# Kernel tuning notes

Measured on AMD Instinct MI355X. Metric: run time of the kernel, lower is better.

The kernel has to match this reference:

```python
import jax, jax.numpy as jnp
import numpy as np

B, L, D = 64, 128, 768          # batch, padded seq len, bert dim
H, HA = 1024, 256               # d_label_hidden, d_label_hidden_arc
POS, V = 18, 40                 # pos vocab, arc (deprel) vocab


def setup_inputs() -> dict:
    key = jax.random.key(0)
    ks = jax.random.split(key, 24)
    n = lambda i, shape, s=0.02: jax.random.normal(ks[i], shape, jnp.float32) * s
    # realistic padding: random sentence lengths in [L//2, L]
    lengths = jax.random.randint(ks[1], (B,), L // 2, L + 1)
    pad_mask = (jnp.arange(L)[None, :] < lengths[:, None]).astype(jnp.float32)
    heads = jax.random.randint(ks[2], (B, L), 0, L)
    # mark padded positions as -1 (zero head vector), as in the original loop
    heads = jnp.where(pad_mask > 0, heads, -1)
    return {
        "ann": jax.random.normal(ks[0], (B, L, D), jnp.float32),
        "pad_mask": pad_mask,
        "correct_heads": heads,
        # label-biaffine branch (hidden H)
        "W_head_mlp": n(3, (D, H)), "b_head_mlp": n(4, (H,)),
        "W_dep_mlp": n(5, (D, H)), "b_dep_mlp": n(6, (H,)),
        "W_lin": n(7, (H, H)), "b_lin": n(8, (H,)),
        "head_vec": n(9, (H,), 1.0), "dep_vec": n(10, (H,), 1.0),
        "bias": n(11, (1, 1, 1), 1.0),
        # arc-label biaffine branch (hidden HA, per-label bilinear)
        "W_head_arc_mlp": n(12, (D, HA)), "b_head_arc_mlp": n(13, (HA,)),
        "W_dep_arc_mlp": n(14, (D, HA)), "b_dep_arc_mlp": n(15, (HA,)),
        "W_arc": n(16, (V, HA, HA), 1.0),
        "head_vec_arc": n(17, (HA, V), 1.0), "dep_vec_arc": n(18, (HA, V), 1.0),
        "bias_arc": n(19, (1, 1, V), 1.0),
        # POS tip
        "W_pos": n(20, (D, POS)), "b_pos": n(21, (POS,)),
    }


def reference(ann, pad_mask, correct_heads,
              W_head_mlp, b_head_mlp, W_dep_mlp, b_dep_mlp,
              W_lin, b_lin, head_vec, dep_vec, bias,
              W_head_arc_mlp, b_head_arc_mlp, W_dep_arc_mlp, b_dep_arc_mlp,
              W_arc, head_vec_arc, dep_vec_arc, bias_arc,
              W_pos, b_pos):
    # POS prediction
    pos_pred = ann @ W_pos + b_pos                                  # [B,L,POS]

    # ---- dependency (unlabeled arc) biaffine ----
    ann_head = jax.nn.relu(ann @ W_head_mlp + b_head_mlp)           # [B,L,H]
    ann_dep = jax.nn.relu(ann @ W_dep_mlp + b_dep_mlp)              # [B,L,H]
    head_bias = ann_head @ head_vec                                 # [B,L]
    dep_bias = ann_dep @ dep_vec                                    # [B,L]
    Wh = ann_head @ W_lin + b_lin                                   # [B,L,H]
    # scores[b,i,j] = dep[b,i] . Wh[b,j]
    dep_W_headT = jnp.einsum('bih,bjh->bij', ann_dep, Wh)
    dep_W_headT = dep_W_headT + head_bias[:, None, :] + dep_bias[:, :, None] + bias
    valid_head = pad_mask[:, None, :] > 0                           # [B,1,L]
    dep_W_headT = jnp.where(valid_head, dep_W_headT, -jnp.inf)

    # ---- labeled arc biaffine (gather gold head per dependent) ----
    ann_head_arc = jax.nn.relu(ann @ W_head_arc_mlp + b_head_arc_mlp)  # [B,L,HA]
    ann_dep_arc = jax.nn.relu(ann @ W_dep_arc_mlp + b_dep_arc_mlp)     # [B,L,HA]
    idx = jnp.clip(correct_heads, 0, L - 1)
    gathered = jnp.take_along_axis(ann_head_arc, idx[:, :, None], axis=1)
    gathered = jnp.where((correct_heads == -1)[:, :, None], 0.0, gathered)  # [B,L,HA]

    head_arc_bias = gathered @ head_vec_arc                         # [B,L,V]
    dep_arc_bias = ann_dep_arc @ dep_vec_arc                        # [B,L,V]
    # per-label bilinear: s[b,l,v] = gathered[b,l] . W_arc[v] . dep[b,l]
    dep_W_headT_arc = jnp.einsum('bld,vde,ble->blv', gathered, W_arc, ann_dep_arc)
    dep_W_headT_arc = dep_W_headT_arc + head_arc_bias + dep_arc_bias + bias_arc

    return pos_pred, dep_W_headT, dep_W_headT_arc
```

## Files before the change

kernel.cpp:

```cpp
#include <hip/hip_runtime.h>
#include <hip/hip_bf16.h>

#define B_ 64
#define L_ 128
#define D_ 768
#define H_ 1024
#define HA_ 256
#define POS_ 18
#define V_ 40
#define BL_ (B_ * L_)

#define NEG_BIG (-1.0e30f)

typedef __attribute__((ext_vector_type(8))) short short8v;
typedef __attribute__((ext_vector_type(4))) short short4v;
typedef __attribute__((ext_vector_type(4))) float f32x4;

__device__ inline void split_bf16(float x, short& hi, short& lo) {
  __hip_bfloat16 h = __float2bfloat16(x);
  hi = *reinterpret_cast<short*>(&h);
  const float r = x - __bfloat162float(h);
  __hip_bfloat16 l = __float2bfloat16(r);
  lo = *reinterpret_cast<short*>(&l);
}

__device__ __forceinline__ short f2b(float x) {
  __hip_bfloat16 h = __float2bfloat16(x);
  return *reinterpret_cast<short*>(&h);
}
__device__ __forceinline__ float b2f(short s) {
  __hip_bfloat16 h = *reinterpret_cast<__hip_bfloat16*>(&s);
  return __bfloat162float(h);
}

__device__ __forceinline__ int swz8(int row, int s) { return ((s + (row >> 1)) & 3) * 8; }
__device__ __forceinline__ int colswz(int row, int n) {
  return (n & ~31) + swz8(row, (n >> 3) & 3) + (n & 7);
}

__device__ __forceinline__ void ld_lds16(const void* g, void* l) {
  __builtin_amdgcn_global_load_lds(
      (const __attribute__((address_space(1))) unsigned int*)g,
      (__attribute__((address_space(3))) unsigned int*)l, 16, 0, 0);
}

template<bool RELU, bool HASBIAS>
__global__ __launch_bounds__(256)
void gemm_bias(const float* __restrict__ A, const float* __restrict__ Bm,
               const float* __restrict__ bias, float* __restrict__ C,
               int M, int N, int K) {
  __shared__ __align__(16) float As[16][68];
  __shared__ __align__(16) float Bs[16][68];
  const int t = threadIdx.x;
  const int tx = t & 15, ty = t >> 4;
  const int m0 = blockIdx.y * 64, n0 = blockIdx.x * 64;
  const int arow = t >> 2, aks = (t & 3) * 4;
  const int bkr = t >> 4, bns = (t & 15) * 4;
  float acc[4][4] = {};
  for (int k0 = 0; k0 < K; k0 += 16) {
    const float4 av = *reinterpret_cast<const float4*>(&A[(size_t)(m0 + arow) * K + k0 + aks]);
    float4 bv;
    const int nb = n0 + bns;
    if (nb + 3 < N) {
      bv = *reinterpret_cast<const float4*>(&Bm[(size_t)(k0 + bkr) * N + nb]);
    } else {
      bv.x = (nb + 0 < N) ? Bm[(size_t)(k0 + bkr) * N + nb + 0] : 0.f;
      bv.y = (nb + 1 < N) ? Bm[(size_t)(k0 + bkr) * N + nb + 1] : 0.f;
      bv.z = (nb + 2 < N) ? Bm[(size_t)(k0 + bkr) * N + nb + 2] : 0.f;
      bv.w = 0.f;
    }
    __syncthreads();
    As[aks + 0][arow] = av.x;
    As[aks + 1][arow] = av.y;
    As[aks + 2][arow] = av.z;
    As[aks + 3][arow] = av.w;
    *reinterpret_cast<float4*>(&Bs[bkr][bns]) = bv;
    __syncthreads();
#pragma unroll
    for (int kk = 0; kk < 16; ++kk) {
      const float4 a4 = *reinterpret_cast<const float4*>(&As[kk][ty * 4]);
      const float4 b4 = *reinterpret_cast<const float4*>(&Bs[kk][tx * 4]);
      const float aa[4] = {a4.x, a4.y, a4.z, a4.w};
      const float bb[4] = {b4.x, b4.y, b4.z, b4.w};
#pragma unroll
      for (int i = 0; i < 4; ++i)
#pragma unroll
        for (int j = 0; j < 4; ++j)
          acc[i][j] = fmaf(aa[i], bb[j], acc[i][j]);
    }
  }
#pragma unroll
  for (int j = 0; j < 4; ++j) {
    const int n = n0 + tx * 4 + j;
    if (n >= N) continue;
    float bj = 0.f;
    if constexpr (HASBIAS) bj = bias[n];
#pragma unroll
    for (int i = 0; i < 4; ++i) {
      const int m = m0 + ty * 4 + i;
      float v = acc[i][j] + bj;
      if (RELU) v = fmaxf(v, 0.f);
      C[(size_t)m * N + n] = v;
    }
  }
}

__global__ __launch_bounds__(256)
void split_pre(const float* __restrict__ src, short* __restrict__ hi,
               short* __restrict__ lo, int K) {
  const int t = threadIdx.x;
  const int r = blockIdx.x * 4 + (t >> 6);
  const int lane = t & 63;
  for (int c = lane * 4; c < K; c += 256) {
    const float4 v = *reinterpret_cast<const float4*>(&src[(size_t)r * K + c]);
    const float vv[4] = {v.x, v.y, v.z, v.w};
    short4v h4, l4;
#pragma unroll
    for (int j = 0; j < 4; ++j) {
      short h, l;
      split_bf16(vv[j], h, l);
      h4[j] = h; l4[j] = l;
    }
    const int cs = colswz(r, c);
    *reinterpret_cast<short4v*>(&hi[(size_t)r * K + cs]) = h4;
    *reinterpret_cast<short4v*>(&lo[(size_t)r * K + cs]) = l4;
  }
}

__global__ __launch_bounds__(256)
void transpose_h(const float* __restrict__ W, short* __restrict__ Thi,
                 int K, int N) {
  __shared__ float tile[32][33];
  const int k0 = blockIdx.y * 32, n0 = blockIdx.x * 32;
  const int t = threadIdx.x;
  const int r = t >> 3, c = (t & 7) * 4;
  const float4 w4 = *reinterpret_cast<const float4*>(&W[(size_t)(k0 + r) * N + n0 + c]);
  tile[r][c + 0] = w4.x;
  tile[r][c + 1] = w4.y;
  tile[r][c + 2] = w4.z;
  tile[r][c + 3] = w4.w;
  __syncthreads();
  short4v hi4;
#pragma unroll
  for (int j = 0; j < 4; ++j) hi4[j] = f2b(tile[c + j][r]);
  const int row = n0 + r;
  const int cs = swz8(row, (c >> 3) & 3) + (c & 7);
  *reinterpret_cast<short4v*>(&Thi[(size_t)row * K + k0 + cs]) = hi4;
}

__global__ __launch_bounds__(256)
void transpose_pos(const float* __restrict__ W, short* __restrict__ Th,
                   short* __restrict__ Tl) {
  const int t = threadIdx.x;
  const int k0 = blockIdx.x * 32;
  const int n = t & 31;
  const int ks = (t >> 5) * 4;
#pragma unroll
  for (int j = 0; j < 4; ++j) {
    const int k = k0 + ks + j;
    const float v = (n < POS_) ? W[(size_t)k * POS_ + n] : 0.f;
    short h, l;
    split_bf16(v, h, l);
    Th[(size_t)n * D_ + colswz(n, k)] = h;
    Tl[(size_t)n * D_ + colswz(n, k)] = l;
  }
}

__global__ __launch_bounds__(256)
void transpose_dv(const float* __restrict__ dv, float* __restrict__ dvT) {
  const int v = blockIdx.x;
  const int e = threadIdx.x;
  dvT[(size_t)v * HA_ + e] = dv[(size_t)e * V_ + v];
}

template<bool STOREBF>
__global__ __launch_bounds__(256)
void gemm_h2(const short* __restrict__ Ath,
             const short* __restrict__ B1t, const short* __restrict__ B2t,
             const float* __restrict__ bias1v, const float* __restrict__ bias2v,
             void* __restrict__ O1, void* __restrict__ O2,
             int M, int N, int K) {
  __shared__ __align__(16) short AhP[2][4096];
  __shared__ __align__(16) short B1P[2][4096];
  __shared__ __align__(16) short B2P[2][4096];
  const int t = threadIdx.x;
  const int lane = t & 63, w = t >> 6;
  const int wm = w >> 1, wn = w & 1;
  const int m0 = blockIdx.y * 128, n0 = blockIdx.x * 128;
  const int fr = lane & 15, kgi = lane >> 4;
  const int drow = lane >> 2, dslot = lane & 3;
  f32x4 acc1[4][4] = {};
  f32x4 acc2[4][4] = {};
  const int nt = K >> 5;

  auto stage = [&](int tt, int pb) {
    const int k0 = tt << 5;
#pragma unroll
    for (int cc = 0; cc < 2; ++cc) {
      const int c = w * 2 + cc;
      const size_t ga = (size_t)(m0 + c * 16 + drow) * K + k0 + dslot * 8;
      ld_lds16(&Ath[ga], &AhP[pb][c * 512]);
      const size_t gb = (size_t)(n0 + c * 16 + drow) * K + k0 + dslot * 8;
      ld_lds16(&B1t[gb], &B1P[pb][c * 512]);
      ld_lds16(&B2t[gb], &B2P[pb][c * 512]);
    }
  };
  auto compute = [&](int pb) {
    short8v ah[4];
#pragma unroll
    for (int mi = 0; mi < 4; ++mi) {
      const int r = wm * 64 + mi * 16 + fr;
      ah[mi] = *reinterpret_cast<const short8v*>(&AhP[pb][r * 32 + swz8(r, kgi)]);
    }
    __builtin_amdgcn_s_setprio(1);
#pragma unroll
    for (int nj = 0; nj < 4; ++nj) {
      const int rn = wn * 64 + nj * 16 + fr;
      const int sw = swz8(rn, kgi);
      const short8v b1 = *reinterpret_cast<const short8v*>(&B1P[pb][rn * 32 + sw]);
      const short8v b2 = *reinterpret_cast<const short8v*>(&B2P[pb][rn * 32 + sw]);
#pragma unroll
      for (int mi = 0; mi < 4; ++mi) {
        acc1[mi][nj] = __builtin_amdgcn_mfma_f32_16x16x32_bf16(ah[mi], b1, acc1[mi][nj], 0, 0, 0);
        acc2[mi][nj] = __builtin_amdgcn_mfma_f32_16x16x32_bf16(ah[mi], b2, acc2[mi][nj], 0, 0, 0);
      }
    }
    __builtin_amdgcn_s_setprio(0);
  };

  stage(0, 0);
  int cur = 0;
  for (int tt = 0; tt < nt; ++tt) {
    if (tt + 1 < nt) {
      stage(tt + 1, cur ^ 1);
      asm volatile("s_waitcnt vmcnt(6)" ::: "memory");
    } else {
      asm volatile("s_waitcnt vmcnt(0)" ::: "memory");
    }
    __builtin_amdgcn_s_barrier();
    compute(cur);
    __builtin_amdgcn_s_barrier();
    cur ^= 1;
  }

  const int rg = lane >> 4;
#pragma unroll
  for (int nj = 0; nj < 4; ++nj) {
    const int n = n0 + wn * 64 + nj * 16 + fr;
    const float b1 = bias1v[n];
    const float b2 = bias2v[n];
#pragma unroll
    for (int mi = 0; mi < 4; ++mi) {
#pragma unroll
      for (int q = 0; q < 4; ++q) {
        const int m = m0 + wm * 64 + mi * 16 + rg * 4 + q;
        float v1 = fmaxf(acc1[mi][nj][q] + b1, 0.f);
        float v2 = fmaxf(acc2[mi][nj][q] + b2, 0.f);
        if constexpr (STOREBF) {
          const size_t o = (size_t)m * N + colswz(m, n);
          ((short*)O1)[o] = f2b(v1);
          ((short*)O2)[o] = f2b(v2);
        } else {
          ((float*)O1)[(size_t)m * N + n] = v1;
          ((float*)O2)[(size_t)m * N + n] = v2;
        }
      }
    }
  }
}

template<bool RELU>
__global__ __launch_bounds__(256)
void gemm_hs(const short* __restrict__ Ath, const short* __restrict__ Bth,
             const float* __restrict__ bias, short* __restrict__ Oh,
             int M, int N, int K) {
  __shared__ __align__(16) short AhP[2][4096];
  __shared__ __align__(16) short BhP[2][4096];
  const int t = threadIdx.x;
  const int lane = t & 63, w = t >> 6;
  const int wm = w >> 1, wn = w & 1;
  const int m0 = blockIdx.y * 128, n0 = blockIdx.x * 128;
  const int fr = lane & 15, kgi = lane >> 4;
  const int drow = lane >> 2, dslot = lane & 3;
  f32x4 acc[4][4] = {};
  const int nt = K >> 5;

  auto stage = [&](int tt, int pb) {
    const int k0 = tt << 5;
#pragma unroll
    for (int cc = 0; cc < 2; ++cc) {
      const int c = w * 2 + cc;
      const size_t ga = (size_t)(m0 + c * 16 + drow) * K + k0 + dslot * 8;
      ld_lds16(&Ath[ga], &AhP[pb][c * 512]);
      const size_t gb = (size_t)(n0 + c * 16 + drow) * K + k0 + dslot * 8;
      ld_lds16(&Bth[gb], &BhP[pb][c * 512]);
    }
  };
  auto compute = [&](int pb) {
    short8v ah[4];
#pragma unroll
    for (int mi = 0; mi < 4; ++mi) {
      const int r = wm * 64 + mi * 16 + fr;
      ah[mi] = *reinterpret_cast<const short8v*>(&AhP[pb][r * 32 + swz8(r, kgi)]);
    }
    __builtin_amdgcn_s_setprio(1);
#pragma unroll
    for (int nj = 0; nj < 4; ++nj) {
      const int rn = wn * 64 + nj * 16 + fr;
      const short8v bh = *reinterpret_cast<const short8v*>(&BhP[pb][rn * 32 + swz8(rn, kgi)]);
#pragma unroll
      for (int mi = 0; mi < 4; ++mi)
        acc[mi][nj] = __builtin_amdgcn_mfma_f32_16x16x32_bf16(ah[mi], bh, acc[mi][nj], 0, 0, 0);
    }
    __builtin_amdgcn_s_setprio(0);
  };

  stage(0, 0);
  int cur = 0;
  for (int tt = 0; tt < nt; ++tt) {
    if (tt + 1 < nt) {
      stage(tt + 1, cur ^ 1);
      asm volatile("s_waitcnt vmcnt(4)" ::: "memory");
    } else {
      asm volatile("s_waitcnt vmcnt(0)" ::: "memory");
    }
    __builtin_amdgcn_s_barrier();
    compute(cur);
    __builtin_amdgcn_s_barrier();
    cur ^= 1;
  }

  const int rg = lane >> 4;
#pragma unroll
  for (int nj = 0; nj < 4; ++nj) {
    const int n = n0 + wn * 64 + nj * 16 + fr;
    const float bj = bias[n];
#pragma unroll
    for (int mi = 0; mi < 4; ++mi) {
#pragma unroll
      for (int q = 0; q < 4; ++q) {
        const int m = m0 + wm * 64 + mi * 16 + rg * 4 + q;
        float v2 = acc[mi][nj][q] + bj;
        if (RELU) v2 = fmaxf(v2, 0.f);
        Oh[(size_t)m * N + colswz(m, n)] = f2b(v2);
      }
    }
  }
}

__global__ __launch_bounds__(256)
void pos_mfma(const short* __restrict__ Ath, const short* __restrict__ Atl,
              const short* __restrict__ Pth, const short* __restrict__ Ptl,
              const float* __restrict__ bias, float* __restrict__ out) {
  extern __shared__ short sm[];
  short* AhP = sm;
  short* AlP = sm + 16384;
  short* BhP = sm + 32768;
  short* BlP = sm + 34816;
  const int t = threadIdx.x;
  const int m0 = blockIdx.x * 256;
  const int lane = t & 63, w = t >> 6;
  const int fr = lane & 15, kgi = lane >> 4;
  const int drow = lane >> 2, dslot = lane & 3;
  f32x4 acc[4][2] = {};

  auto stage = [&](int tt, int pb) {
    const int k0 = tt << 5;
#pragma unroll
    for (int cc = 0; cc < 4; ++cc) {
      const int c = w * 4 + cc;
      const size_t ga = (size_t)(m0 + c * 16 + drow) * D_ + k0 + dslot * 8;
      ld_lds16(&Ath[ga], &AhP[pb * 8192 + c * 512]);
      ld_lds16(&Atl[ga], &AlP[pb * 8192 + c * 512]);
    }
    {
      const short* bsrc = (w & 2) ? Ptl : Pth;
      short* bdst = (w & 2) ? BlP : BhP;
      const int c = w & 1;
      const size_t gb = (size_t)(c * 16 + drow) * D_ + k0 + dslot * 8;
      ld_lds16(&bsrc[gb], &bdst[pb * 1024 + c * 512]);
    }
  };
  auto compute = [&](int pb) {
    short8v ah[4], al[4];
#pragma unroll
    for (int mi = 0; mi < 4; ++mi) {
      const int r = w * 64 + mi * 16 + fr;
      const int sw = swz8(r, kgi);
      ah[mi] = *reinterpret_cast<const short8v*>(&AhP[pb * 8192 + r * 32 + sw]);
      al[mi] = *reinterpret_cast<const short8v*>(&AlP[pb * 8192 + r * 32 + sw]);
    }
#pragma unroll
    for (int nj = 0; nj < 2; ++nj) {
      const int rn = nj * 16 + fr;
      const int sw = swz8(rn, kgi);
      const short8v bh = *reinterpret_cast<const short8v*>(&BhP[pb * 1024 + rn * 32 + sw]);
      const short8v bl = *reinterpret_cast<const short8v*>(&BlP[pb * 1024 + rn * 32 + sw]);
#pragma unroll
      for (int mi = 0; mi < 4; ++mi) {
        acc[mi][nj] = __builtin_amdgcn_mfma_f32_16x16x32_bf16(ah[mi], bh, acc[mi][nj], 0, 0, 0);
        acc[mi][nj] = __builtin_amdgcn_mfma_f32_16x16x32_bf16(al[mi], bh, acc[mi][nj], 0, 0, 0);
        acc[mi][nj] = __builtin_amdgcn_mfma_f32_16x16x32_bf16(ah[mi], bl, acc[mi][nj], 0, 0, 0);
      }
    }
  };

  stage(0, 0);
  int cur = 0;
  for (int tt = 0; tt < 24; ++tt) {
    if (tt + 1 < 24) {
      stage(tt + 1, cur ^ 1);
      asm volatile("s_waitcnt vmcnt(9)" ::: "memory");
    } else {
      asm volatile("s_waitcnt vmcnt(0)" ::: "memory");
    }
    __builtin_amdgcn_s_barrier();
    compute(cur);
    __builtin_amdgcn_s_barrier();
    cur ^= 1;
  }

  const int rg = lane >> 4;
#pragma unroll
  for (int nj = 0; nj < 2; ++nj) {
    const int n = nj * 16 + fr;
    if (n >= POS_) continue;
    const float bj = bias[n];
#pragma unroll
    for (int mi = 0; mi < 4; ++mi) {
#pragma unroll
      for (int q = 0; q < 4; ++q) {
        const int m = m0 + w * 64 + mi * 16 + rg * 4 + q;
        out[(size_t)m * POS_ + n] = acc[mi][nj][q] + bj;
      }
    }
  }
}

__global__ __launch_bounds__(256)
void bias_dots_h(const short* __restrict__ Ahh, const short* __restrict__ Adh,
                 const float* __restrict__ head_vec, const float* __restrict__ dep_vec,
                 float* __restrict__ hb, float* __restrict__ db) {
  const int t = threadIdx.x;
  const int m = blockIdx.x * 4 + (t >> 6);
  const int lane = t & 63;
  float sh = 0.f, sd = 0.f;
#pragma unroll
  for (int jj = 0; jj < 4; ++jj) {
    const int c = lane * 16 + jj * 4;
    const size_t o = (size_t)m * H_ + colswz(m, c);
    const short4v h4 = *reinterpret_cast<const short4v*>(&Ahh[o]);
    const short4v d4 = *reinterpret_cast<const short4v*>(&Adh[o]);
    const float4 hv = *reinterpret_cast<const float4*>(&head_vec[c]);
    const float4 dv = *reinterpret_cast<const float4*>(&dep_vec[c]);
    const float hvv[4] = {hv.x, hv.y, hv.z, hv.w};
    const float dvv[4] = {dv.x, dv.y, dv.z, dv.w};
#pragma unroll
    for (int j = 0; j < 4; ++j) {
      sh = fmaf(b2f(h4[j]), hvv[j], sh);
      sd = fmaf(b2f(d4[j]), dvv[j], sd);
    }
  }
#pragma unroll
  for (int off = 32; off; off >>= 1) {
    sh += __shfl_xor(sh, off);
    sd += __shfl_xor(sd, off);
  }
  if (lane == 0) {
    hb[m] = sh;
    db[m] = sd;
  }
}

__global__ __launch_bounds__(256)
void scores_h(const short* __restrict__ Adh, const short* __restrict__ Whh,
              const float* __restrict__ hb, const float* __restrict__ db,
              const float* __restrict__ pad_mask, const float* __restrict__ bias1,
              float* __restrict__ out2) {
  __shared__ __align__(16) short AhP[2][2048];
  __shared__ __align__(16) short BhP[2][2048];
  const int t = threadIdx.x;
  const int b = blockIdx.z;
  const int i0 = blockIdx.y * 64, j0 = blockIdx.x * 64;
  const int lane = t & 63, w = t >> 6;
  const int wm = w >> 1, wn = w & 1;
  const int fr = lane & 15, kgi = lane >> 4;
  const int drow = lane >> 2, dslot = lane & 3;
  const size_t abase = ((size_t)b * L_ + i0) * H_;
  const size_t bbase = ((size_t)b * L_ + j0) * H_;
  f32x4 acc[2][2] = {};

  auto stage = [&](int tt, int pb) {
    const int k0 = tt << 5;
    const size_t ga = abase + (size_t)(w * 16 + drow) * H_ + k0 + dslot * 8;
    ld_lds16(&Adh[ga], &AhP[pb][w * 512]);
    const size_t gb = bbase + (size_t)(w * 16 + drow) * H_ + k0 + dslot * 8;
    ld_lds16(&Whh[gb], &BhP[pb][w * 512]);
  };
  auto compute = [&](int pb) {
    short8v ah[2];
#pragma unroll
    for (int mi = 0; mi < 2; ++mi) {
      const int r = wm * 32 + mi * 16 + fr;
      ah[mi] = *reinterpret_cast<const short8v*>(&AhP[pb][r * 32 + swz8(r, kgi)]);
    }
    __builtin_amdgcn_s_setprio(1);
#pragma unroll
    for (int nj = 0; nj < 2; ++nj) {
      const int rn = wn * 32 + nj * 16 + fr;
      const short8v bh = *reinterpret_cast<const short8v*>(&BhP[pb][rn * 32 + swz8(rn, kgi)]);
#pragma unroll
      for (int mi = 0; mi < 2; ++mi)
        acc[mi][nj] = __builtin_amdgcn_mfma_f32_16x16x32_bf16(ah[mi], bh, acc[mi][nj], 0, 0, 0);
    }
    __builtin_amdgcn_s_setprio(0);
  };

  stage(0, 0);
  int cur = 0;
  for (int tt = 0; tt < 32; ++tt) {
    if (tt + 1 < 32) {
      stage(tt + 1, cur ^ 1);
      asm volatile("s_waitcnt vmcnt(2)" ::: "memory");
    } else {
      asm volatile("s_waitcnt vmcnt(0)" ::: "memory");
    }
    __builtin_amdgcn_s_barrier();
    compute(cur);
    __builtin_amdgcn_s_barrier();
    cur ^= 1;
  }

  const int rg = lane >> 4;
  const float bias0 = bias1[0];
#pragma unroll
  for (int nj = 0; nj < 2; ++nj) {
    const int jcol = j0 + wn * 32 + nj * 16 + fr;
    const float mj = pad_mask[b * L_ + jcol];
    const float hbj = hb[b * L_ + jcol];
#pragma unroll
    for (int mi = 0; mi < 2; ++mi) {
#pragma unroll
      for (int q = 0; q < 4; ++q) {
        const int irow = i0 + wm * 32 + mi * 16 + rg * 4 + q;
        float v = acc[mi][nj][q] + hbj + db[b * L_ + irow] + bias0;
        if (!(mj > 0.f)) v = NEG_BIG;
        out2[((size_t)b * L_ + irow) * L_ + jcol] = v;
      }
    }
  }
}

__global__ __launch_bounds__(256)
void transposeW_h(const float* __restrict__ W, short* __restrict__ Whi) {
  __shared__ float tile[32][33];
  const int v = blockIdx.z, d0 = blockIdx.y * 32, e0 = blockIdx.x * 32;
  const int t = threadIdx.x;
  const int r = t >> 3, c = (t & 7) * 4;
  const float4 w4 = *reinterpret_cast<const float4*>(
      &W[((size_t)v * HA_ + d0 + r) * HA_ + e0 + c]);
  tile[r][c + 0] = w4.x;
  tile[r][c + 1] = w4.y;
  tile[r][c + 2] = w4.z;
  tile[r][c + 3] = w4.w;
  __syncthreads();
  short4v hi4;
#pragma unroll
  for (int j = 0; j < 4; ++j) hi4[j] = f2b(tile[c + j][r]);
  const int row = e0 + r;
  const int cs = swz8(row, (c >> 3) & 3) + (c & 7);
  *reinterpret_cast<short4v*>(&Whi[((size_t)v * HA_ + row) * HA_ + d0 + cs]) = hi4;
}

__global__ __launch_bounds__(256)
void gather_h(const float* __restrict__ head_arcb, const int* __restrict__ heads,
              float* __restrict__ g32, short* __restrict__ g_hi) {
  const int t = threadIdx.x;
  const int m = blockIdx.x * 4 + (t >> 6);
  const int lane = t & 63;
  const int h = heads[m];
  float4 g4 = make_float4(0.f, 0.f, 0.f, 0.f);
  if (h >= 0)
    g4 = *reinterpret_cast<const float4*>(
        &head_arcb[((size_t)((m >> 7) * L_ + h)) * HA_ + lane * 4]);
  *reinterpret_cast<float4*>(&g32[(size_t)m * HA_ + lane * 4]) = g4;
  short4v hi4;
  const float gv[4] = {g4.x, g4.y, g4.z, g4.w};
#pragma unroll
  for (int j = 0; j < 4; ++j) hi4[j] = f2b(gv[j]);
  *reinterpret_cast<short4v*>(&g_hi[(size_t)m * HA_ + colswz(m, lane * 4)]) = hi4;
}

__global__ __launch_bounds__(512)
void arc_h(const short* __restrict__ g_hi, const short* __restrict__ Wt_hi,
           const float* __restrict__ dep32, const float* __restrict__ hb_arc,
           const float* __restrict__ dvT, float* __restrict__ out3) {
  __shared__ __align__(16) short AhP[2][8192];
  __shared__ __align__(16) short BhP[2][8192];
  __shared__ float parts[256][2];
  const int t = threadIdx.x;
  const int bid = blockIdx.x;
  const int xcd = bid & 7;
  const int j = bid >> 3;
  const int m0 = (j / 5) * 256;
  const int v = xcd * 5 + (j % 5);
  const int lane = t & 63, w = t >> 6;
  const int wm = w >> 1, we = w & 1;
  const int fr = lane & 15, kgi = lane >> 4;
  const int drow = lane >> 2, dslot = lane & 3;
  const size_t wbase = (size_t)v * HA_ * HA_;

  f32x4 acc[4][8] = {};

  auto stage = [&](int tt, int pb) {
    const int k0 = tt << 5;
#pragma unroll
    for (int cc = 0; cc < 2; ++cc) {
      const int c = w * 2 + cc;
      const size_t ga = (size_t)(m0 + c * 16 + drow) * HA_ + k0 + dslot * 8;
      ld_lds16(&g_hi[ga], &AhP[pb][c * 512]);
      const size_t gb = wbase + (size_t)(c * 16 + drow) * HA_ + k0 + dslot * 8;
      ld_lds16(&Wt_hi[gb], &BhP[pb][c * 512]);
    }
  };
  auto compute = [&](int pb) {
    short8v ah[4];
#pragma unroll
    for (int mi = 0; mi < 4; ++mi) {
      const int r = wm * 64 + mi * 16 + fr;
      ah[mi] = *reinterpret_cast<const short8v*>(&AhP[pb][r * 32 + swz8(r, kgi)]);
    }
    __builtin_amdgcn_s_setprio(1);
#pragma unroll
    for (int ej = 0; ej < 8; ++ej) {
      const int rb = we * 128 + ej * 16 + fr;
      const short8v bh = *reinterpret_cast<const short8v*>(&BhP[pb][rb * 32 + swz8(rb, kgi)]);
#pragma unroll
      for (int mi = 0; mi < 4; ++mi)
        acc[mi][ej] = __builtin_amdgcn_mfma_f32_16x16x32_bf16(ah[mi], bh, acc[mi][ej], 0, 0, 0);
    }
    __builtin_amdgcn_s_setprio(0);
  };

  stage(0, 0);
  int cur = 0;
#pragma unroll
  for (int tt = 0; tt < 8; ++tt) {
    if (tt < 7) {
      stage(tt + 1, cur ^ 1);
      asm volatile("s_waitcnt vmcnt(4)" ::: "memory");
    } else {
      asm volatile("s_waitcnt vmcnt(0)" ::: "memory");
    }
    __builtin_amdgcn_s_barrier();
    compute(cur);
    __builtin_amdgcn_s_barrier();
    cur ^= 1;
  }

  const int rg = lane >> 4;
  float dvr[8];
#pragma unroll
  for (int ej = 0; ej < 8; ++ej)
    dvr[ej] = dvT[(size_t)v * HA_ + we * 128 + ej * 16 + fr];
#pragma unroll
  for (int mi = 0; mi < 4; ++mi) {
#pragma unroll
    for (int q = 0; q < 4; ++q) {
      const int mrow = wm * 64 + mi * 16 + rg * 4 + q;
      const int m = m0 + mrow;
      float s = 0.f;
#pragma unroll
      for (int ej = 0; ej < 8; ++ej)
        s = fmaf(acc[mi][ej][q] + dvr[ej],
                 dep32[(size_t)m * HA_ + we * 128 + ej * 16 + fr], s);
      s += __shfl_xor(s, 1, 16);
      s += __shfl_xor(s, 2, 16);
      s += __shfl_xor(s, 4, 16);
      s += __shfl_xor(s, 8, 16);
      if (fr == 0) parts[mrow][we] = s;
    }
  }
  __syncthreads();
  if (t < 256) {
    const int m = m0 + t;
    out3[(size_t)m * V_ + v] = parts[t][0] + parts[t][1] + hb_arc[(size_t)m * V_ + v];
  }
}

extern "C" void kernel_launch(void* const* d_in, const int* in_sizes, int n_in,
                              void* d_out, int out_size, void* d_ws, size_t ws_size,
                              hipStream_t stream) {
  const float* ann        = (const float*)d_in[0];
  const float* pad_mask   = (const float*)d_in[1];
  const int*   heads      = (const int*)d_in[2];
  const float* W_head_mlp = (const float*)d_in[3];
  const float* b_head_mlp = (const float*)d_in[4];
  const float* W_dep_mlp  = (const float*)d_in[5];
  const float* b_dep_mlp  = (const float*)d_in[6];
  const float* W_lin      = (const float*)d_in[7];
  const float* b_lin      = (const float*)d_in[8];
  const float* head_vec   = (const float*)d_in[9];
  const float* dep_vec    = (const float*)d_in[10];
  const float* bias1      = (const float*)d_in[11];
  const float* W_head_arc = (const float*)d_in[12];
  const float* b_head_arc = (const float*)d_in[13];
  const float* W_dep_arc  = (const float*)d_in[14];
  const float* b_dep_arc  = (const float*)d_in[15];
  const float* W_arc      = (const float*)d_in[16];
  const float* hv_arc     = (const float*)d_in[17];
  const float* dv_arc     = (const float*)d_in[18];
  const float* bias_arc   = (const float*)d_in[19];
  const float* W_pos      = (const float*)d_in[20];
  const float* b_pos      = (const float*)d_in[21];

  float* out_pos    = (float*)d_out;
  float* out_scores = out_pos + (size_t)BL_ * POS_;
  float* out_arc    = out_scores + (size_t)B_ * L_ * L_;

  float* ws  = (float*)d_ws;
  float* R1  = ws;
  float* R2  = R1 + (size_t)BL_ * H_;
  float* R3  = R2 + (size_t)BL_ * H_;
  float* head_arcb = R3 + (size_t)BL_ * H_;
  float* dep_arcb  = head_arcb + (size_t)BL_ * HA_;
  float* hb        = dep_arcb + (size_t)BL_ * HA_;
  float* db        = hb + BL_;
  short* wt0     = (short*)(db + BL_);
  short* Wth_hm  = wt0;
  short* Wth_dm  = Wth_hm + (size_t)H_ * D_;
  short* Wth_lin = Wth_dm + (size_t)H_ * D_;
  short* Wth_ha  = Wth_lin + (size_t)H_ * H_;
  short* Wth_da  = Wth_ha + (size_t)HA_ * D_;
  short* Pth     = Wth_da + (size_t)HA_ * D_;
  short* Ptl     = Pth + (size_t)32 * D_;
  short* Ahh = (short*)R1;
  short* Adh = (short*)R2;
  short* Ath = (short*)R3;  short* Atl = Ath + (size_t)BL_ * D_;
  short* Whh = (short*)R3;
  float* g32 = (float*)wt0;
  short* Wt_hi  = (short*)R1;
  short* g_hi   = Wt_hi + (size_t)V_ * HA_ * HA_;
  float* hb_arc = (float*)(g_hi + (size_t)BL_ * HA_);
  float* dvT    = hb_arc + (size_t)BL_ * V_;

  hipFuncSetAttribute((const void*)pos_mfma, hipFuncAttributeMaxDynamicSharedMemorySize, 73728);

  const dim3 blk(256);
  split_pre<<<dim3(BL_ / 4), blk, 0, stream>>>(ann, Ath, Atl, D_);
  transpose_h<<<dim3(H_ / 32, D_ / 32), blk, 0, stream>>>(W_head_mlp, Wth_hm, D_, H_);
  transpose_h<<<dim3(H_ / 32, D_ / 32), blk, 0, stream>>>(W_dep_mlp, Wth_dm, D_, H_);
  transpose_h<<<dim3(H_ / 32, H_ / 32), blk, 0, stream>>>(W_lin, Wth_lin, H_, H_);
  transpose_h<<<dim3(HA_ / 32, D_ / 32), blk, 0, stream>>>(W_head_arc, Wth_ha, D_, HA_);
  transpose_h<<<dim3(HA_ / 32, D_ / 32), blk, 0, stream>>>(W_dep_arc, Wth_da, D_, HA_);
  transpose_pos<<<dim3(D_ / 32), blk, 0, stream>>>(W_pos, Pth, Ptl);

  gemm_h2<true><<<dim3(H_ / 128, BL_ / 128), blk, 0, stream>>>(
      Ath, Wth_hm, Wth_dm, b_head_mlp, b_dep_mlp, Ahh, Adh, BL_, H_, D_);
  gemm_h2<false><<<dim3(HA_ / 128, BL_ / 128), blk, 0, stream>>>(
      Ath, Wth_ha, Wth_da, b_head_arc, b_dep_arc, head_arcb, dep_arcb, BL_, HA_, D_);
  pos_mfma<<<dim3(BL_ / 256), blk, 73728, stream>>>(Ath, Atl, Pth, Ptl, b_pos, out_pos);
  gemm_hs<false><<<dim3(H_ / 128, BL_ / 128), blk, 0, stream>>>(
      Ahh, Wth_lin, b_lin, Whh, BL_, H_, H_);

  bias_dots_h<<<dim3(BL_ / 4), blk, 0, stream>>>(Ahh, Adh, head_vec, dep_vec, hb, db);
  scores_h<<<dim3(2, 2, B_), blk, 0, stream>>>(
      Adh, Whh, hb, db, pad_mask, bias1, out_scores);

  transposeW_h<<<dim3(HA_ / 32, HA_ / 32, V_), blk, 0, stream>>>(W_arc, Wt_hi);
  transpose_dv<<<dim3(V_), blk, 0, stream>>>(dv_arc, dvT);
  gather_h<<<dim3(BL_ / 4), blk, 0, stream>>>(head_arcb, heads, g32, g_hi);
  gemm_bias<false, true><<<dim3(1, BL_ / 64), blk, 0, stream>>>(
      g32, hv_arc, bias_arc, hb_arc, BL_, V_, HA_);
  arc_h<<<dim3((BL_ / 256) * V_), dim3(512), 0, stream>>>(
      g_hi, Wt_hi, dep_arcb, hb_arc, dvT, out_arc);
}
```

Before: 290.1 us.

## Merge weight-prep, dual MLP GEMMs and arc-prep kernels into fewer launches

Five weight transposes plus the POS transpose become one megaprep kernel that dispatches on block index. The two gemm_h2 instantiations (H and HA outputs) are merged into one 640-block launch, and the W_arc transpose, dv transpose and head gather become one arcprep kernel. This removes about eight kernel launches and the tail gaps between them, and lets small grids fill the GPU together. In exchange there is extra runtime branching, and the merged GEMM loses its compile-time store-type specialization.

```diff
diff --git a/kernel.cpp b/kernel.cpp
--- a/kernel.cpp
+++ b/kernel.cpp
@@ -128,79 +128,92 @@
 }
 
 __global__ __launch_bounds__(256)
-void transpose_h(const float* __restrict__ W, short* __restrict__ Thi,
-                 int K, int N) {
+void megaprep(const float* __restrict__ Whm, const float* __restrict__ Wdm,
+              const float* __restrict__ Wlin, const float* __restrict__ Wha,
+              const float* __restrict__ Wda, const float* __restrict__ Wpos,
+              short* __restrict__ Thm, short* __restrict__ Tdm,
+              short* __restrict__ Tlin, short* __restrict__ Tha,
+              short* __restrict__ Tda, short* __restrict__ Pth,
+              short* __restrict__ Ptl) {
   __shared__ float tile[32][33];
-  const int k0 = blockIdx.y * 32, n0 = blockIdx.x * 32;
-  const int t = threadIdx.x;
-  const int r = t >> 3, c = (t & 7) * 4;
-  const float4 w4 = *reinterpret_cast<const float4*>(&W[(size_t)(k0 + r) * N + n0 + c]);
-  tile[r][c + 0] = w4.x;
-  tile[r][c + 1] = w4.y;
-  tile[r][c + 2] = w4.z;
-  tile[r][c + 3] = w4.w;
-  __syncthreads();
-  short4v hi4;
-#pragma unroll
-  for (int j = 0; j < 4; ++j) hi4[j] = f2b(tile[c + j][r]);
-  const int row = n0 + r;
-  const int cs = swz8(row, (c >> 3) & 3) + (c & 7);
-  *reinterpret_cast<short4v*>(&Thi[(size_t)row * K + k0 + cs]) = hi4;
-}
-
-__global__ __launch_bounds__(256)
-void transpose_pos(const float* __restrict__ W, short* __restrict__ Th,
-                   short* __restrict__ Tl) {
-  const int t = threadIdx.x;
-  const int k0 = blockIdx.x * 32;
-  const int n = t & 31;
-  const int ks = (t >> 5) * 4;
-#pragma unroll
-  for (int j = 0; j < 4; ++j) {
-    const int k = k0 + ks + j;
-    const float v = (n < POS_) ? W[(size_t)k * POS_ + n] : 0.f;
-    short h, l;
-    split_bf16(v, h, l);
-    Th[(size_t)n * D_ + colswz(n, k)] = h;
-    Tl[(size_t)n * D_ + colswz(n, k)] = l;
-  }
-}
-
-__global__ __launch_bounds__(256)
-void transpose_dv(const float* __restrict__ dv, float* __restrict__ dvT) {
-  const int v = blockIdx.x;
-  const int e = threadIdx.x;
-  dvT[(size_t)v * HA_ + e] = dv[(size_t)e * V_ + v];
-}
-
-template<bool STOREBF>
-__global__ __launch_bounds__(256)
-void gemm_h2(const short* __restrict__ Ath,
-             const short* __restrict__ B1t, const short* __restrict__ B2t,
-             const float* __restrict__ bias1v, const float* __restrict__ bias2v,
-             void* __restrict__ O1, void* __restrict__ O2,
-             int M, int N, int K) {
+  const int bid = blockIdx.x;
+  const int t = threadIdx.x;
+  if (bid < 2944) {
+    const float* W; short* T; int K, N, local;
+    if (bid < 768)       { W = Whm;  T = Thm;  K = D_; N = H_;  local = bid; }
+    else if (bid < 1536) { W = Wdm;  T = Tdm;  K = D_; N = H_;  local = bid - 768; }
+    else if (bid < 2560) { W = Wlin; T = Tlin; K = H_; N = H_;  local = bid - 1536; }
+    else if (bid < 2752) { W = Wha;  T = Tha;  K = D_; N = HA_; local = bid - 2560; }
+    else                 { W = Wda;  T = Tda;  K = D_; N = HA_; local = bid - 2752; }
+    const int ntiles = N >> 5;
+    const int n0 = (local % ntiles) * 32;
+    const int k0 = (local / ntiles) * 32;
+    const int r = t >> 3, c = (t & 7) * 4;
+    const float4 w4 = *reinterpret_cast<const float4*>(&W[(size_t)(k0 + r) * N + n0 + c]);
+    tile[r][c + 0] = w4.x;
+    tile[r][c + 1] = w4.y;
+    tile[r][c + 2] = w4.z;
+    tile[r][c + 3] = w4.w;
+    __syncthreads();
+    short4v hi4;
+#pragma unroll
+    for (int j = 0; j < 4; ++j) hi4[j] = f2b(tile[c + j][r]);
+    const int row = n0 + r;
+    const int cs = swz8(row, (c >> 3) & 3) + (c & 7);
+    *reinterpret_cast<short4v*>(&T[(size_t)row * K + k0 + cs]) = hi4;
+  } else {
+    const int k0 = (bid - 2944) * 32;
+    const int n = t & 31;
+    const int ks = (t >> 5) * 4;
+#pragma unroll
+    for (int j = 0; j < 4; ++j) {
+      const int k = k0 + ks + j;
+      const float v = (n < POS_) ? Wpos[(size_t)k * POS_ + n] : 0.f;
+      short h, l;
+      split_bf16(v, h, l);
+      Pth[(size_t)n * D_ + colswz(n, k)] = h;
+      Ptl[(size_t)n * D_ + colswz(n, k)] = l;
+    }
+  }
+}
+
+__global__ __launch_bounds__(256)
+void gemm_h2x(const short* __restrict__ Ath,
+              const short* __restrict__ B1h, const short* __restrict__ B2h,
+              const float* __restrict__ bias1h, const float* __restrict__ bias2h,
+              short* __restrict__ O1h, short* __restrict__ O2h,
+              const short* __restrict__ B1a, const short* __restrict__ B2a,
+              const float* __restrict__ bias1a, const float* __restrict__ bias2a,
+              float* __restrict__ O1a, float* __restrict__ O2a) {
   __shared__ __align__(16) short AhP[2][4096];
   __shared__ __align__(16) short B1P[2][4096];
   __shared__ __align__(16) short B2P[2][4096];
+  const int bid = blockIdx.x;
+  const bool big = bid < 512;
+  const int N = big ? H_ : HA_;
+  const int ntx = N >> 7;
+  const int local = big ? bid : bid - 512;
+  const int m0 = (local / ntx) * 128, n0 = (local % ntx) * 128;
+  const short* B1t = big ? B1h : B1a;
+  const short* B2t = big ? B2h : B2a;
+  const float* bias1v = big ? bias1h : bias1a;
+  const float* bias2v = big ? bias2h : bias2a;
   const int t = threadIdx.x;
   const int lane = t & 63, w = t >> 6;
   const int wm = w >> 1, wn = w & 1;
-  const int m0 = blockIdx.y * 128, n0 = blockIdx.x * 128;
   const int fr = lane & 15, kgi = lane >> 4;
   const int drow = lane >> 2, dslot = lane & 3;
   f32x4 acc1[4][4] = {};
   f32x4 acc2[4][4] = {};
-  const int nt = K >> 5;
 
   auto stage = [&](int tt, int pb) {
     const int k0 = tt << 5;
 #pragma unroll
     for (int cc = 0; cc < 2; ++cc) {
       const int c = w * 2 + cc;
-      const size_t ga = (size_t)(m0 + c * 16 + drow) * K + k0 + dslot * 8;
+      const size_t ga = (size_t)(m0 + c * 16 + drow) * D_ + k0 + dslot * 8;
       ld_lds16(&Ath[ga], &AhP[pb][c * 512]);
-      const size_t gb = (size_t)(n0 + c * 16 + drow) * K + k0 + dslot * 8;
+      const size_t gb = (size_t)(n0 + c * 16 + drow) * D_ + k0 + dslot * 8;
       ld_lds16(&B1t[gb], &B1P[pb][c * 512]);
       ld_lds16(&B2t[gb], &B2P[pb][c * 512]);
     }
@@ -230,8 +243,8 @@
 
   stage(0, 0);
   int cur = 0;
-  for (int tt = 0; tt < nt; ++tt) {
-    if (tt + 1 < nt) {
+  for (int tt = 0; tt < 24; ++tt) {
+    if (tt + 1 < 24) {
       stage(tt + 1, cur ^ 1);
       asm volatile("s_waitcnt vmcnt(6)" ::: "memory");
     } else {
@@ -254,15 +267,15 @@
 #pragma unroll
       for (int q = 0; q < 4; ++q) {
         const int m = m0 + wm * 64 + mi * 16 + rg * 4 + q;
-        float v1 = fmaxf(acc1[mi][nj][q] + b1, 0.f);
-        float v2 = fmaxf(acc2[mi][nj][q] + b2, 0.f);
-        if constexpr (STOREBF) {
+        const float v1 = fmaxf(acc1[mi][nj][q] + b1, 0.f);
+        const float v2 = fmaxf(acc2[mi][nj][q] + b2, 0.f);
+        if (big) {
           const size_t o = (size_t)m * N + colswz(m, n);
-          ((short*)O1)[o] = f2b(v1);
-          ((short*)O2)[o] = f2b(v2);
+          O1h[o] = f2b(v1);
+          O2h[o] = f2b(v2);
         } else {
-          ((float*)O1)[(size_t)m * N + n] = v1;
-          ((float*)O2)[(size_t)m * N + n] = v2;
+          O1a[(size_t)m * N + n] = v1;
+          O2a[(size_t)m * N + n] = v2;
         }
       }
     }
@@ -552,43 +565,48 @@
 }
 
 __global__ __launch_bounds__(256)
-void transposeW_h(const float* __restrict__ W, short* __restrict__ Whi) {
+void arcprep(const float* __restrict__ Warc, const float* __restrict__ dv,
+             const float* __restrict__ head_arcb, const int* __restrict__ heads,
+             short* __restrict__ WtA, float* __restrict__ dvT,
+             float* __restrict__ g32, short* __restrict__ g_hi) {
   __shared__ float tile[32][33];
-  const int v = blockIdx.z, d0 = blockIdx.y * 32, e0 = blockIdx.x * 32;
-  const int t = threadIdx.x;
-  const int r = t >> 3, c = (t & 7) * 4;
-  const float4 w4 = *reinterpret_cast<const float4*>(
-      &W[((size_t)v * HA_ + d0 + r) * HA_ + e0 + c]);
-  tile[r][c + 0] = w4.x;
-  tile[r][c + 1] = w4.y;
-  tile[r][c + 2] = w4.z;
-  tile[r][c + 3] = w4.w;
-  __syncthreads();
-  short4v hi4;
-#pragma unroll
-  for (int j = 0; j < 4; ++j) hi4[j] = f2b(tile[c + j][r]);
-  const int row = e0 + r;
-  const int cs = swz8(row, (c >> 3) & 3) + (c & 7);
-  *reinterpret_cast<short4v*>(&Whi[((size_t)v * HA_ + row) * HA_ + d0 + cs]) = hi4;
-}
-
-__global__ __launch_bounds__(256)
-void gather_h(const float* __restrict__ head_arcb, const int* __restrict__ heads,
-              float* __restrict__ g32, short* __restrict__ g_hi) {
-  const int t = threadIdx.x;
-  const int m = blockIdx.x * 4 + (t >> 6);
-  const int lane = t & 63;
-  const int h = heads[m];
-  float4 g4 = make_float4(0.f, 0.f, 0.f, 0.f);
-  if (h >= 0)
-    g4 = *reinterpret_cast<const float4*>(
-        &head_arcb[((size_t)((m >> 7) * L_ + h)) * HA_ + lane * 4]);
-  *reinterpret_cast<float4*>(&g32[(size_t)m * HA_ + lane * 4]) = g4;
-  short4v hi4;
-  const float gv[4] = {g4.x, g4.y, g4.z, g4.w};
-#pragma unroll
-  for (int j = 0; j < 4; ++j) hi4[j] = f2b(gv[j]);
-  *reinterpret_cast<short4v*>(&g_hi[(size_t)m * HA_ + colswz(m, lane * 4)]) = hi4;
+  const int bid = blockIdx.x;
+  const int t = threadIdx.x;
+  if (bid < 2560) {
+    const int v = bid >> 6, rem = bid & 63;
+    const int d0 = (rem >> 3) * 32, e0 = (rem & 7) * 32;
+    const int r = t >> 3, c = (t & 7) * 4;
+    const float4 w4 = *reinterpret_cast<const float4*>(
+        &Warc[((size_t)v * HA_ + d0 + r) * HA_ + e0 + c]);
+    tile[r][c + 0] = w4.x;
+    tile[r][c + 1] = w4.y;
+    tile[r][c + 2] = w4.z;
+    tile[r][c + 3] = w4.w;
+    __syncthreads();
+    short4v hi4;
+#pragma unroll
+    for (int j = 0; j < 4; ++j) hi4[j] = f2b(tile[c + j][r]);
+    const int row = e0 + r;
+    const int cs = swz8(row, (c >> 3) & 3) + (c & 7);
+    *reinterpret_cast<short4v*>(&WtA[((size_t)v * HA_ + row) * HA_ + d0 + cs]) = hi4;
+  } else if (bid < 2600) {
+    const int v = bid - 2560;
+    dvT[(size_t)v * HA_ + t] = dv[(size_t)t * V_ + v];
+  } else {
+    const int m = (bid - 2600) * 4 + (t >> 6);
+    const int lane = t & 63;
+    const int h = heads[m];
+    float4 g4 = make_float4(0.f, 0.f, 0.f, 0.f);
+    if (h >= 0)
+      g4 = *reinterpret_cast<const float4*>(
+          &head_arcb[((size_t)((m >> 7) * L_ + h)) * HA_ + lane * 4]);
+    *reinterpret_cast<float4*>(&g32[(size_t)m * HA_ + lane * 4]) = g4;
+    short4v hi4;
+    const float gv[4] = {g4.x, g4.y, g4.z, g4.w};
+#pragma unroll
+    for (int j = 0; j < 4; ++j) hi4[j] = f2b(gv[j]);
+    *reinterpret_cast<short4v*>(&g_hi[(size_t)m * HA_ + colswz(m, lane * 4)]) = hi4;
+  }
 }
 
 __global__ __launch_bounds__(512)
@@ -748,17 +766,13 @@
 
   const dim3 blk(256);
   split_pre<<<dim3(BL_ / 4), blk, 0, stream>>>(ann, Ath, Atl, D_);
-  transpose_h<<<dim3(H_ / 32, D_ / 32), blk, 0, stream>>>(W_head_mlp, Wth_hm, D_, H_);
-  transpose_h<<<dim3(H_ / 32, D_ / 32), blk, 0, stream>>>(W_dep_mlp, Wth_dm, D_, H_);
-  transpose_h<<<dim3(H_ / 32, H_ / 32), blk, 0, stream>>>(W_lin, Wth_lin, H_, H_);
-  transpose_h<<<dim3(HA_ / 32, D_ / 32), blk, 0, stream>>>(W_head_arc, Wth_ha, D_, HA_);
-  transpose_h<<<dim3(HA_ / 32, D_ / 32), blk, 0, stream>>>(W_dep_arc, Wth_da, D_, HA_);
-  transpose_pos<<<dim3(D_ / 32), blk, 0, stream>>>(W_pos, Pth, Ptl);
-
-  gemm_h2<true><<<dim3(H_ / 128, BL_ / 128), blk, 0, stream>>>(
-      Ath, Wth_hm, Wth_dm, b_head_mlp, b_dep_mlp, Ahh, Adh, BL_, H_, D_);
-  gemm_h2<false><<<dim3(HA_ / 128, BL_ / 128), blk, 0, stream>>>(
-      Ath, Wth_ha, Wth_da, b_head_arc, b_dep_arc, head_arcb, dep_arcb, BL_, HA_, D_);
+  megaprep<<<dim3(2968), blk, 0, stream>>>(
+      W_head_mlp, W_dep_mlp, W_lin, W_head_arc, W_dep_arc, W_pos,
+      Wth_hm, Wth_dm, Wth_lin, Wth_ha, Wth_da, Pth, Ptl);
+
+  gemm_h2x<<<dim3(640), blk, 0, stream>>>(
+      Ath, Wth_hm, Wth_dm, b_head_mlp, b_dep_mlp, Ahh, Adh,
+      Wth_ha, Wth_da, b_head_arc, b_dep_arc, head_arcb, dep_arcb);
   pos_mfma<<<dim3(BL_ / 256), blk, 73728, stream>>>(Ath, Atl, Pth, Ptl, b_pos, out_pos);
   gemm_hs<false><<<dim3(H_ / 128, BL_ / 128), blk, 0, stream>>>(
       Ahh, Wth_lin, b_lin, Whh, BL_, H_, H_);
@@ -767,9 +781,8 @@
   scores_h<<<dim3(2, 2, B_), blk, 0, stream>>>(
       Adh, Whh, hb, db, pad_mask, bias1, out_scores);
 
-  transposeW_h<<<dim3(HA_ / 32, HA_ / 32, V_), blk, 0, stream>>>(W_arc, Wt_hi);
-  transpose_dv<<<dim3(V_), blk, 0, stream>>>(dv_arc, dvT);
-  gather_h<<<dim3(BL_ / 4), blk, 0, stream>>>(head_arcb, heads, g32, g_hi);
+  arcprep<<<dim3(4648), blk, 0, stream>>>(
+      W_arc, dv_arc, head_arcb, heads, Wt_hi, dvT, g32, g_hi);
   gemm_bias<false, true><<<dim3(1, BL_ / 64), blk, 0, stream>>>(
       g32, hv_arc, bias_arc, hb_arc, BL_, V_, HA_);
   arc_h<<<dim3((BL_ / 256) * V_), dim3(512), 0, stream>>>(
```

Result: no change. 294.4 us (+1.5%).
